# Kernel tuning notes

Hardware: AMD Instinct MI355X
Metric: run time of the kernel (lower is better)

Reference implementation:

```python
import jax, jax.numpy as jnp
import numpy as np

# Model dims (match init_kwargs)
D_OUT = 64      # d_in == d_out
SEQ_L = 4096    # input_len
K_EIG = 24      # num_eigh
K_U = 3         # auto_reg_k_u
K_Y = 2         # auto_reg_k_y
BATCH = 8


def get_top_hankel_eigh(n, k):
    """Top-k eigenpairs of the Hankel matrix Z[i,j] = 2/((i+j)^3-(i+j)), 1-indexed."""
    idx = np.arange(1, n + 1, dtype=np.float64)
    s = idx[:, None] + idx[None, :]
    z = 2.0 / (s ** 3 - s)
    vals, vecs = np.linalg.eigh(z)  # ascending
    return (jnp.asarray(vals[-k:], jnp.float32),        # [k]
            jnp.asarray(vecs[:, -k:], jnp.float32))     # [n, k]


def setup_inputs() -> dict:
    key = jax.random.key(0)
    k1, k2, k3, k4 = jax.random.split(key, 4)
    eig_vals, eig_vecs = get_top_hankel_eigh(SEQ_L, K_EIG)
    m_x_var = 1.0 / float(D_OUT) ** 0.5
    return {
        "inputs": jax.random.normal(k1, (BATCH, SEQ_L, D_OUT), jnp.float32),
        "m_y": jax.random.normal(k2, (D_OUT, K_Y, D_OUT), jnp.float32) * 0.01,
        "m_u": jax.random.normal(k3, (D_OUT, D_OUT, K_U), jnp.float32) * m_x_var,
        "m_phi": jax.random.normal(k4, (D_OUT * K_EIG, D_OUT), jnp.float32) * 0.01,
        "eig_vals": eig_vals,
        "eig_vecs": eig_vecs,
    }


def _stu_single(x, m_y, m_u, m_phi, eig_vals, eig_vecs):
    """apply_stu for one sequence x: [L, d] -> [L, d]."""
    L, d = x.shape
    n = 2 * L
    # --- compute_x_tilde: causal FFT conv of each eigenvector with each channel ---
    V = jnp.fft.rfft(eig_vecs, n=n, axis=0)             # [F, k]
    U = jnp.fft.rfft(x, n=n, axis=0)                    # [F, d]
    xt = jnp.fft.irfft(V[:, :, None] * U[:, None, :], n=n, axis=0)[:L]  # [L, k, d]
    xt = xt * (eig_vals ** 0.25)[None, :, None]
    x_tilde = xt.reshape(L, K_EIG * d)                  # [L, k*d]
    # --- delta_phi ---
    delta_phi = jnp.einsum('lk,kd->ld', x_tilde, m_phi)  # [L, d_out]
    # --- compute_ar_x_preds: shifted AR input contributions ---
    o = jnp.einsum('oik,li->klo', m_u, x)               # [k_u, L, d_out]
    shifts = jnp.arange(K_U)
    o = jax.vmap(lambda a, i: jnp.roll(a, i, axis=0))(o, shifts)
    mask = (jnp.arange(L)[None, :] >= shifts[:, None]).astype(x.dtype)  # [k_u, L]
    delta_ar_u = jnp.sum(o * mask[:, :, None], axis=0)  # [L, d_out]
    deltas = delta_phi + delta_ar_u
    # --- compute_y_t: sequential AR recurrence over time ---
    def step(carry, dlt):  # carry: [k_y, d_out]
        out = jnp.tensordot(m_y, carry, axes=2) + dlt    # [d_out]
        carry = jnp.roll(carry, 1, axis=0).at[0].set(out)
        return carry, out
    _, ys = jax.lax.scan(step, jnp.zeros((K_Y, d), x.dtype), deltas)
    return ys  # [L, d_out]


def reference(inputs, m_y, m_u, m_phi, eig_vals, eig_vecs):
    return jax.vmap(lambda x: _stu_single(x, m_y, m_u, m_phi, eig_vals, eig_vecs))(inputs)
```

## Files before the change

kernel.cpp:

```cpp
#include <hip/hip_runtime.h>
#include <math.h>

#define BB 8
#define LL 4096
#define DD 64
#define KK 24
#define KT 27
#define NN 8192
#define LOGN 13
#define NP 4128
#define NCH 256
#define CH 16
#define PAD 80

typedef unsigned int uint;
typedef unsigned short u16;
typedef __attribute__((ext_vector_type(8))) short bf16x8;
typedef __attribute__((ext_vector_type(4))) float f32x4;

__device__ __forceinline__ float bfl(uint u) {
    union { uint u; float f; } v; v.u = u << 16; return v.f;
}
__device__ __forceinline__ float bfh(uint u) {
    union { uint u; float f; } v; v.u = u & 0xFFFF0000u; return v.f;
}
__device__ __forceinline__ uint pk(float x) {
    union { float f; uint u; } v; v.f = x;
    return (v.u + 0x7FFFu + ((v.u >> 16) & 1u)) >> 16;
}
__device__ __forceinline__ float2 unpk2(uint u) {
    return make_float2(bfl(u), bfh(u));
}
__device__ __forceinline__ int br13(int v) { return (int)(__brev((uint)v) >> 19); }

template<int NT>
__device__ __forceinline__ void build_tw(float2* twc) {
    const int tid = threadIdx.x;
    for (int i = tid; i < 8192; i += NT) {
        if (i == 0) { twc[0] = make_float2(1.f, 0.f); continue; }
        int lh = 31 - __builtin_clz((uint)i);
        int j = i - (1 << lh);
        float ang = -6.28318530717958647692f * (float)j / (float)(2 << lh);
        float sn, cs;
        __sincosf(ang, &sn, &cs);
        twc[i] = make_float2(cs, sn);
    }
}

template<int NT>
__device__ __forceinline__ void fft_dif(float2* a, const float2* __restrict__ twc) {
    const int tid = threadIdx.x;
    for (int lh = LOGN - 1; lh >= 0; --lh) {
        const int half = 1 << lh;
#pragma unroll
        for (int bb = 0; bb < NN / 2 / NT; ++bb) {
            int t = tid + bb * NT;
            int j = t & (half - 1);
            int i0 = ((t >> lh) << (lh + 1)) + j;
            float2 u = a[i0], v = a[i0 + half];
            float2 w = twc[half + j];
            float cs = w.x, sn = w.y;
            float dx = u.x - v.x, dy = u.y - v.y;
            a[i0] = make_float2(u.x + v.x, u.y + v.y);
            a[i0 + half] = make_float2(dx * cs - dy * sn, dx * sn + dy * cs);
        }
        __syncthreads();
    }
}

template<int NT>
__device__ __forceinline__ void fft_dit(float2* a, const float2* __restrict__ twc) {
    const int tid = threadIdx.x;
    for (int lh = 0; lh < LOGN; ++lh) {
        const int half = 1 << lh;
#pragma unroll
        for (int bb = 0; bb < NN / 2 / NT; ++bb) {
            int t = tid + bb * NT;
            int j = t & (half - 1);
            int i0 = ((t >> lh) << (lh + 1)) + j;
            float2 u = a[i0], v = a[i0 + half];
            float2 w = twc[half + j];
            float cs = w.x, sn = -w.y;
            float wx = v.x * cs - v.y * sn;
            float wy = v.x * sn + v.y * cs;
            a[i0] = make_float2(u.x + wx, u.y + wy);
            a[i0 + half] = make_float2(u.x - wx, u.y - wy);
        }
        __syncthreads();
    }
}


__global__ __launch_bounds__(256) void k_pack(const float* __restrict__ mphi,
                                              const float* __restrict__ mu,
                                              uint* __restrict__ mp2) {
    int idx = blockIdx.x * 256 + threadIdx.x;
    if (idx >= KT * 2048) return;
    int k = idx >> 11;
    int rem = idx & 2047;
    int o = rem >> 5, cp = rem & 31;
    int c = cp * 2;
    uint v;
    if (k < KK) {
        v = pk(mphi[(k * 64 + c) * 64 + o]) | (pk(mphi[(k * 64 + c + 1) * 64 + o]) << 16);
    } else {
        int ku = k - KK;
        v = pk(mu[(o * 64 + c) * 3 + ku]) | (pk(mu[(o * 64 + c + 1) * 3 + ku]) << 16);
    }
    mp2[idx] = v;
}

__global__ __launch_bounds__(256) void k_fft_filters(const float* __restrict__ eig_vals,
                                                     const float* __restrict__ eig_vecs,
                                                     float2* __restrict__ Vb) {
    __shared__ float2 a[NN];
    __shared__ float2 twc[8192];
    const int k = blockIdx.x, tid = threadIdx.x;
    const float alpha = powf(eig_vals[k], 0.25f) * (1.0f / (float)NN);
    for (int t = tid; t < LL; t += 256)
        a[t] = make_float2(eig_vecs[t * KK + k] * alpha, 0.f);
    for (int t = LL + tid; t < NN; t += 256)
        a[t] = make_float2(0.f, 0.f);
    build_tw<256>(twc);
    __syncthreads();
    fft_dif<256>(a, twc);
    for (int r = tid; r < NN; r += 256)
        Vb[(size_t)r * KK + k] = a[r];
}

__global__ __launch_bounds__(512) void k_fft_x2(const float* __restrict__ x,
                                                uint* __restrict__ Uxp,
                                                uint* __restrict__ Uyp) {
    __shared__ float2 a[NN];
    __shared__ float2 twc[8192];
    const int b = blockIdx.x & 7, cp = blockIdx.x >> 3;
    const int tid = threadIdx.x;
    for (int l = tid; l < LL; l += 512)
        a[l] = *(const float2*)&x[((size_t)b * LL + l) * DD + 2 * cp];
    for (int l = LL + tid; l < NN; l += 512)
        a[l] = make_float2(0.f, 0.f);
    build_tw<512>(twc);
    __syncthreads();
    fft_dif<512>(a, twc);
    const size_t plane = ((size_t)b * 32 + cp) * NP;
    for (int idx = tid; idx < 4097; idx += 512) {
        int r = (idx == 4096) ? 1 : 2 * idx;
        int fn = br13(r);
        int q = br13((8192 - fn) & 8191);
        float2 Z = a[r], W = a[q];
        float ucx = 0.5f * (Z.x + W.x), ucy = 0.5f * (Z.y - W.y);
        float upx = 0.5f * (Z.y + W.y), upy = 0.5f * (W.x - Z.x);
        Uxp[plane + idx] = pk(ucx) | (pk(upx) << 16);
        Uyp[plane + idx] = pk(ucy) | (pk(upy) << 16);
    }
    for (int idx = 4097 + tid; idx < NP; idx += 512) {
        Uxp[plane + idx] = 0;
        Uyp[plane + idx] = 0;
    }
}

__global__ __launch_bounds__(256) void k_modulate5(const float2* __restrict__ Vb,
                                                   const uint* __restrict__ Uxp,
                                                   const uint* __restrict__ Uyp,
                                                   const uint* __restrict__ mp2,
                                                   uint* __restrict__ Sb2) {
    __shared__ u16 Uxs[32][PAD];
    __shared__ u16 Uys[32][PAD];
    __shared__ u16 mpT[2][64][PAD];
    __shared__ float2 Vt[32][28];
    const int tid = threadIdx.x;
    const int pt = blockIdx.x;
    const int b  = blockIdx.y;
    const int p0 = pt * 32;

    for (int i = tid; i < 1024; i += 256) {
        int cp = i >> 5, row = i & 31;
        uint vx = Uxp[((size_t)b * 32 + cp) * NP + p0 + row];
        uint vy = Uyp[((size_t)b * 32 + cp) * NP + p0 + row];
        *(uint*)&Uxs[row][cp * 2] = vx;
        *(uint*)&Uys[row][cp * 2] = vy;
    }
    {
        int o = tid >> 2, seg = tid & 3;
        const uint4* src = (const uint4*)&mp2[(size_t)o * 32 + seg * 8];
        uint4 m0 = src[0], m1 = src[1];
        *(uint4*)&mpT[0][o][seg * 16] = m0;
        *(uint4*)&mpT[0][o][seg * 16 + 8] = m1;
    }
    for (int i = tid; i < 768; i += 256) {
        int pi = i / 24, kk = i - pi * 24;
        int pidx = p0 + pi; if (pidx > 4096) pidx = 4096;
        int r = (pidx == 4096) ? 1 : 2 * pidx;
        Vt[pi][kk] = Vb[(size_t)r * KK + kk];
    }
    for (int pi = tid; pi < 32; pi += 256) {
        int pidx = p0 + pi; if (pidx > 4096) pidx = 4096;
        int r = (pidx == 4096) ? 1 : 2 * pidx;
        int f = br13(r);
        const float invN = 1.f / 8192.f;
        float ph = -6.28318530717958647692f * (float)f * invN;
        float s1, c1, s2, c2;
        __sincosf(ph, &s1, &c1);
        __sincosf(2.f * ph, &s2, &c2);
        Vt[pi][24] = make_float2(invN, 0.f);
        Vt[pi][25] = make_float2(c1 * invN, s1 * invN);
        Vt[pi][26] = make_float2(c2 * invN, s2 * invN);
    }
    __syncthreads();

    const int lane = tid & 63, w = tid >> 6;
    const int rt = w & 1, chalf = w >> 1;
    const int lrow = lane & 15, lk = lane >> 4;
    const u16* axp = &Uxs[rt * 16 + lrow][lk * 8];
    const u16* ayp = &Uys[rt * 16 + lrow][lk * 8];

    float Sx0[4] = {0.f, 0.f, 0.f, 0.f}, Sy0[4] = {0.f, 0.f, 0.f, 0.f};
    float Sx1[4] = {0.f, 0.f, 0.f, 0.f}, Sy1[4] = {0.f, 0.f, 0.f, 0.f};

    for (int k = 0; k < KT; ++k) {
        const int cur = k & 1;
        bf16x8 ax0 = *(const bf16x8*)(axp);
        bf16x8 ax1 = *(const bf16x8*)(axp + 32);
        bf16x8 ay0 = *(const bf16x8*)(ayp);
        bf16x8 ay1 = *(const bf16x8*)(ayp + 32);
        const u16* bp0 = &mpT[cur][chalf * 32 + lrow][lk * 8];
        const u16* bp1 = &mpT[cur][chalf * 32 + 16 + lrow][lk * 8];
        bf16x8 b00 = *(const bf16x8*)(bp0);
        bf16x8 b01 = *(const bf16x8*)(bp0 + 32);
        bf16x8 b10 = *(const bf16x8*)(bp1);
        bf16x8 b11 = *(const bf16x8*)(bp1 + 32);
        float2 v0 = Vt[rt * 16 + lk * 4 + 0][k];
        float2 v1 = Vt[rt * 16 + lk * 4 + 1][k];
        float2 v2 = Vt[rt * 16 + lk * 4 + 2][k];
        float2 v3 = Vt[rt * 16 + lk * 4 + 3][k];
        if (k + 1 < KT) {
            int o = tid >> 2, seg = tid & 3;
            const uint4* src = (const uint4*)&mp2[((size_t)(k + 1) * 64 + o) * 32 + seg * 8];
            uint4 m0 = src[0], m1 = src[1];
            *(uint4*)&mpT[cur ^ 1][o][seg * 16] = m0;
            *(uint4*)&mpT[cur ^ 1][o][seg * 16 + 8] = m1;
        }
        f32x4 z = {0.f, 0.f, 0.f, 0.f};
        f32x4 Wx0 = __builtin_amdgcn_mfma_f32_16x16x32_bf16(ax0, b00, z, 0, 0, 0);
        Wx0 = __builtin_amdgcn_mfma_f32_16x16x32_bf16(ax1, b01, Wx0, 0, 0, 0);
        f32x4 Wy0 = __builtin_amdgcn_mfma_f32_16x16x32_bf16(ay0, b00, z, 0, 0, 0);
        Wy0 = __builtin_amdgcn_mfma_f32_16x16x32_bf16(ay1, b01, Wy0, 0, 0, 0);
        f32x4 Wx1 = __builtin_amdgcn_mfma_f32_16x16x32_bf16(ax0, b10, z, 0, 0, 0);
        Wx1 = __builtin_amdgcn_mfma_f32_16x16x32_bf16(ax1, b11, Wx1, 0, 0, 0);
        f32x4 Wy1 = __builtin_amdgcn_mfma_f32_16x16x32_bf16(ay0, b10, z, 0, 0, 0);
        Wy1 = __builtin_amdgcn_mfma_f32_16x16x32_bf16(ay1, b11, Wy1, 0, 0, 0);
        Sx0[0] += v0.x * Wx0[0] - v0.y * Wy0[0];  Sy0[0] += v0.x * Wy0[0] + v0.y * Wx0[0];
        Sx0[1] += v1.x * Wx0[1] - v1.y * Wy0[1];  Sy0[1] += v1.x * Wy0[1] + v1.y * Wx0[1];
        Sx0[2] += v2.x * Wx0[2] - v2.y * Wy0[2];  Sy0[2] += v2.x * Wy0[2] + v2.y * Wx0[2];
        Sx0[3] += v3.x * Wx0[3] - v3.y * Wy0[3];  Sy0[3] += v3.x * Wy0[3] + v3.y * Wx0[3];
        Sx1[0] += v0.x * Wx1[0] - v0.y * Wy1[0];  Sy1[0] += v0.x * Wy1[0] + v0.y * Wx1[0];
        Sx1[1] += v1.x * Wx1[1] - v1.y * Wy1[1];  Sy1[1] += v1.x * Wy1[1] + v1.y * Wx1[1];
        Sx1[2] += v2.x * Wx1[2] - v2.y * Wy1[2];  Sy1[2] += v2.x * Wy1[2] + v2.y * Wx1[2];
        Sx1[3] += v3.x * Wx1[3] - v3.y * Wy1[3];  Sy1[3] += v3.x * Wy1[3] + v3.y * Wx1[3];
        __syncthreads();
    }
    const int rbase = rt * 16 + lk * 4;
    const int o0 = chalf * 32 + lrow;
    const size_t pl0 = ((size_t)b * 64 + o0) * NP + p0 + rbase;
    const size_t pl1 = ((size_t)b * 64 + o0 + 16) * NP + p0 + rbase;
#pragma unroll
    for (int j = 0; j < 4; ++j) {
        Sb2[pl0 + j] = pk(Sx0[j]) | (pk(Sy0[j]) << 16);
        Sb2[pl1 + j] = pk(Sx1[j]) | (pk(Sy1[j]) << 16);
    }
}

__global__ __launch_bounds__(512) void k_ifft2(const uint* __restrict__ Sb2,
                                               float* __restrict__ deltas) {
    __shared__ float2 a[NN];
    __shared__ float2 twc[8192];
    const int b = blockIdx.x & 7, op = blockIdx.x >> 3;
    const int tid = threadIdx.x;
    const uint* s0 = &Sb2[((size_t)b * 64 + op * 2) * NP];
    const uint* s1 = &Sb2[((size_t)b * 64 + op * 2 + 1) * NP];
    for (int idx = tid; idx < 4097; idx += 512) {
        int r = (idx == 4096) ? 1 : 2 * idx;
        float2 A = unpk2(s0[idx]), B = unpk2(s1[idx]);
        a[r] = make_float2(A.x - B.y, A.y + B.x);
        int fn = br13(r);
        int q = br13((8192 - fn) & 8191);
        if (q != r) a[q] = make_float2(A.x + B.y, B.x - A.y);
    }
    build_tw<512>(twc);
    __syncthreads();
    fft_dit<512>(a, twc);
    float* d0 = &deltas[((size_t)b * 64 + op * 2) * LL];
    float* d1 = &deltas[((size_t)b * 64 + op * 2 + 1) * LL];
    for (int l = tid; l < LL; l += 512) {
        d0[l] = a[l].x;
        d1[l] = a[l].y;
    }
}

__global__ __launch_bounds__(256) void k_matsq1(const float* __restrict__ m_y,
                                                float* __restrict__ C) {
    int idx = blockIdx.x * 256 + threadIdx.x;
    int r = idx >> 7, c = idx & 127;
    if (r >= 64) { C[idx] = m_y[(r - 64) * 128 + c]; return; }
    float acc = (c < 64) ? m_y[r * 128 + 64 + c] : 0.f;
#pragma unroll
    for (int i = 0; i < 64; ++i) acc += m_y[r * 128 + i] * m_y[i * 128 + c];
    C[idx] = acc;
}

__global__ __launch_bounds__(256) void k_matsq(const float* __restrict__ A,
                                               float* __restrict__ C) {
    int idx = blockIdx.x * 256 + threadIdx.x;
    int r = idx >> 7, c = idx & 127;
    float acc = 0.f;
#pragma unroll
    for (int i = 0; i < 128; ++i) acc += A[r * 128 + i] * A[i * 128 + c];
    C[idx] = acc;
}

__device__ __forceinline__ void load_rowhalf(const float* __restrict__ P, int r, int h,
                                             float* __restrict__ p) {
#pragma unroll
    for (int i4 = 0; i4 < 16; ++i4) {
        float4 v = *(const float4*)&P[r * 128 + h * 64 + i4 * 4];
        p[4 * i4] = v.x; p[4 * i4 + 1] = v.y; p[4 * i4 + 2] = v.z; p[4 * i4 + 3] = v.w;
    }
}
__device__ __forceinline__ float dot64(const float* __restrict__ p, const float* s) {
    float a0 = 0.f, a1 = 0.f, a2 = 0.f, a3 = 0.f;
#pragma unroll
    for (int i4 = 0; i4 < 16; ++i4) {
        float4 w = *(const float4*)&s[i4 * 4];
        a0 += p[4 * i4] * w.x;  a1 += p[4 * i4 + 1] * w.y;
        a2 += p[4 * i4 + 2] * w.z;  a3 += p[4 * i4 + 3] * w.w;
    }
    return (a0 + a1) + (a2 + a3);
}

__global__ __launch_bounds__(256, 1) void k_scan(const float* __restrict__ P,
                                                 const float* __restrict__ in,
                                                 float* __restrict__ partial,
                                                 float* __restrict__ terminal,
                                                 const int count) {
    const int bx = blockIdx.x;
    const int tid = threadIdx.x;
    const int r = tid & 127, h = tid >> 7;
    __shared__ __align__(16) float scur[128];
    __shared__ float pacc[256];
    float p[64];
    load_rowhalf(P, r, h, p);
    if (tid < 128) scur[tid] = 0.f;
    __syncthreads();
    const size_t base = (size_t)bx * count * 128;
    for (int k = 0; k < count; ++k) {
        if (tid < 128) partial[base + (size_t)k * 128 + tid] = scur[tid];
        pacc[tid] = dot64(p, &scur[h * 64]);
        __syncthreads();
        if (tid < 128) scur[tid] = pacc[tid] + pacc[tid + 128] + in[base + (size_t)k * 128 + tid];
        __syncthreads();
    }
    if (tid < 128) terminal[(size_t)bx * 128 + tid] = scur[tid];
}

__global__ __launch_bounds__(256, 1) void k_fixupg(const float* __restrict__ P,
                                                   const float* __restrict__ Sinit,
                                                   const float* __restrict__ q,
                                                   float* __restrict__ out,
                                                   const int count) {
    const int bx = blockIdx.x;
    const int tid = threadIdx.x;
    const int r = tid & 127, h = tid >> 7;
    __shared__ __align__(16) float scur[128];
    __shared__ float pacc[256];
    float p[64];
    load_rowhalf(P, r, h, p);
    if (tid < 128) scur[tid] = Sinit[(size_t)bx * 128 + tid];
    __syncthreads();
    const size_t base = (size_t)bx * count * 128;
    for (int k = 0; k < count; ++k) {
        if (tid < 128) out[base + (size_t)k * 128 + tid] = scur[tid] + q[base + (size_t)k * 128 + tid];
        if (k == count - 1) break;
        pacc[tid] = dot64(p, &scur[h * 64]);
        __syncthreads();
        if (tid < 128) scur[tid] = pacc[tid] + pacc[tid + 128];
        __syncthreads();
    }
}

__global__ __launch_bounds__(128, 1) void k_chunk_local(const float* __restrict__ deltas,
                                                        const float* __restrict__ m_y,
                                                        float* __restrict__ term) {
    const int b = blockIdx.x >> 8, j = blockIdx.x & 255;
    const int tid = threadIdx.x;
    const int o = tid & 63, h = tid >> 6;
    __shared__ __align__(16) float y1s[64];
    __shared__ __align__(16) float y2s[64];
    __shared__ float pacc[128];
    float m1[32], m2[32];
#pragma unroll
    for (int i4 = 0; i4 < 8; ++i4) {
        float4 v1 = *(const float4*)&m_y[o * 128 + h * 32 + i4 * 4];
        float4 v2 = *(const float4*)&m_y[o * 128 + 64 + h * 32 + i4 * 4];
        m1[4 * i4] = v1.x; m1[4 * i4 + 1] = v1.y; m1[4 * i4 + 2] = v1.z; m1[4 * i4 + 3] = v1.w;
        m2[4 * i4] = v2.x; m2[4 * i4 + 1] = v2.y; m2[4 * i4 + 2] = v2.z; m2[4 * i4 + 3] = v2.w;
    }
    if (tid < 64) { y1s[tid] = 0.f; y2s[tid] = 0.f; }
    __syncthreads();
    const float* dl = &deltas[((size_t)b * 64 + o) * LL + j * CH];
    for (int t = 0; t < CH; ++t) {
        float a0 = 0.f, a1 = 0.f, a2 = 0.f, a3 = 0.f;
#pragma unroll
        for (int i4 = 0; i4 < 8; ++i4) {
            float4 w1 = *(const float4*)&y1s[h * 32 + i4 * 4];
            float4 w2 = *(const float4*)&y2s[h * 32 + i4 * 4];
            a0 += m1[4 * i4] * w1.x + m2[4 * i4] * w2.x;
            a1 += m1[4 * i4 + 1] * w1.y + m2[4 * i4 + 1] * w2.y;
            a2 += m1[4 * i4 + 2] * w1.z + m2[4 * i4 + 2] * w2.z;
            a3 += m1[4 * i4 + 3] * w1.w + m2[4 * i4 + 3] * w2.w;
        }
        pacc[tid] = (a0 + a1) + (a2 + a3);
        __syncthreads();
        if (h == 0) {
            float outv = pacc[o] + pacc[o + 64] + dl[t];
            y2s[o] = y1s[o];
            y1s[o] = outv;
        }
        __syncthreads();
    }
    if (tid < 64) {
        term[((size_t)b * NCH + j) * 128 + o] = y1s[o];
        term[((size_t)b * NCH + j) * 128 + 64 + o] = y2s[o];
    }
}

__global__ __launch_bounds__(128, 1) void k_chunk_final(const float* __restrict__ deltas,
                                                        const float* __restrict__ m_y,
                                                        const float* __restrict__ sstate,
                                                        float* __restrict__ out) {
    const int b = blockIdx.x >> 8, j = blockIdx.x & 255;
    const int tid = threadIdx.x;
    const int o = tid & 63, h = tid >> 6;
    __shared__ __align__(16) float y1s[64];
    __shared__ __align__(16) float y2s[64];
    __shared__ float pacc[128];
    float m1[32], m2[32];
#pragma unroll
    for (int i4 = 0; i4 < 8; ++i4) {
        float4 v1 = *(const float4*)&m_y[o * 128 + h * 32 + i4 * 4];
        float4 v2 = *(const float4*)&m_y[o * 128 + 64 + h * 32 + i4 * 4];
        m1[4 * i4] = v1.x; m1[4 * i4 + 1] = v1.y; m1[4 * i4 + 2] = v1.z; m1[4 * i4 + 3] = v1.w;
        m2[4 * i4] = v2.x; m2[4 * i4 + 1] = v2.y; m2[4 * i4 + 2] = v2.z; m2[4 * i4 + 3] = v2.w;
    }
    if (tid < 64) {
        y1s[tid] = sstate[((size_t)b * NCH + j) * 128 + tid];
        y2s[tid] = sstate[((size_t)b * NCH + j) * 128 + 64 + tid];
    }
    __syncthreads();
    const float* dl = &deltas[((size_t)b * 64 + o) * LL + j * CH];
    const size_t obase = (((size_t)b * LL) + j * CH) * DD + o;
    for (int t = 0; t < CH; ++t) {
        float a0 = 0.f, a1 = 0.f, a2 = 0.f, a3 = 0.f;
#pragma unroll
        for (int i4 = 0; i4 < 8; ++i4) {
            float4 w1 = *(const float4*)&y1s[h * 32 + i4 * 4];
            float4 w2 = *(const float4*)&y2s[h * 32 + i4 * 4];
            a0 += m1[4 * i4] * w1.x + m2[4 * i4] * w2.x;
            a1 += m1[4 * i4 + 1] * w1.y + m2[4 * i4 + 1] * w2.y;
            a2 += m1[4 * i4 + 2] * w1.z + m2[4 * i4 + 2] * w2.z;
            a3 += m1[4 * i4 + 3] * w1.w + m2[4 * i4 + 3] * w2.w;
        }
        pacc[tid] = (a0 + a1) + (a2 + a3);
        __syncthreads();
        if (h == 0) {
            float outv = pacc[o] + pacc[o + 64] + dl[t];
            out[obase + (size_t)t * DD] = outv;
            y2s[o] = y1s[o];
            y1s[o] = outv;
        }
        __syncthreads();
    }
}

extern "C" void kernel_launch(void* const* d_in, const int* in_sizes, int n_in,
                              void* d_out, int out_size, void* d_ws, size_t ws_size,
                              hipStream_t stream) {
    const float* x        = (const float*)d_in[0];
    const float* m_y      = (const float*)d_in[1];
    const float* m_u      = (const float*)d_in[2];
    const float* m_phi    = (const float*)d_in[3];
    const float* eig_vals = (const float*)d_in[4];
    const float* eig_vecs = (const float*)d_in[5];
    float* out = (float*)d_out;

    char* ws = (char*)d_ws;
    size_t off = 0;
    auto alloc = [&](size_t bytes) -> void* {
        void* p = ws + off;
        off += (bytes + 255) & ~(size_t)255;
        return p;
    };
    float2* Vb   = (float2*)alloc((size_t)NN * KK * sizeof(float2));
    uint*   Uxp  = (uint*)alloc((size_t)BB * 32 * NP * sizeof(uint));
    uint*   Uyp  = (uint*)alloc((size_t)BB * 32 * NP * sizeof(uint));
    uint*   Sb2  = (uint*)alloc((size_t)BB * 64 * NP * sizeof(uint));
    float*  deltas = (float*)alloc((size_t)BB * 64 * LL * sizeof(float));
    uint*   mp2  = (uint*)alloc((size_t)KT * 64 * 32 * sizeof(uint));
    float*  mats = (float*)alloc((size_t)5 * 128 * 128 * sizeof(float));
    float*  term = (float*)alloc((size_t)BB * NCH * 128 * sizeof(float));
    float*  sst  = (float*)alloc((size_t)BB * NCH * 128 * sizeof(float));
    float*  qbuf = (float*)alloc((size_t)BB * NCH * 128 * sizeof(float));
    float*  Qg   = (float*)alloc((size_t)BB * 32 * 128 * sizeof(float));
    float*  q2   = (float*)alloc((size_t)BB * 32 * 128 * sizeof(float));
    float*  Sgt  = (float*)alloc((size_t)BB * 32 * 128 * sizeof(float));
    float*  Qsg  = (float*)alloc((size_t)BB * 4 * 128 * sizeof(float));
    float*  Ssg  = (float*)alloc((size_t)BB * 4 * 128 * sizeof(float));
    float*  dmy  = (float*)alloc((size_t)8 * 128 * sizeof(float));

    k_pack<<<dim3(216), dim3(256), 0, stream>>>(m_phi, m_u, mp2);
    k_fft_filters<<<dim3(24), dim3(256), 0, stream>>>(eig_vals, eig_vecs, Vb);
    k_fft_x2<<<dim3(256), dim3(512), 0, stream>>>(x, Uxp, Uyp);

    float* T1    = mats;
    float* T2    = mats + 16384;
    float* P16   = mats + 32768;
    float* P128  = mats + 49152;
    float* P1024 = mats + 65536;
    k_matsq1<<<dim3(64), dim3(256), 0, stream>>>(m_y, T1);
    k_matsq<<<dim3(64), dim3(256), 0, stream>>>(T1, T2);
    k_matsq<<<dim3(64), dim3(256), 0, stream>>>(T2, T1);
    k_matsq<<<dim3(64), dim3(256), 0, stream>>>(T1, P16);
    k_matsq<<<dim3(64), dim3(256), 0, stream>>>(P16, T1);
    k_matsq<<<dim3(64), dim3(256), 0, stream>>>(T1, T2);
    k_matsq<<<dim3(64), dim3(256), 0, stream>>>(T2, P128);
    k_matsq<<<dim3(64), dim3(256), 0, stream>>>(P128, T1);
    k_matsq<<<dim3(64), dim3(256), 0, stream>>>(T1, T2);
    k_matsq<<<dim3(64), dim3(256), 0, stream>>>(T2, P1024);

    k_modulate5<<<dim3(129, 8), dim3(256), 0, stream>>>(Vb, Uxp, Uyp, mp2, Sb2);
    k_ifft2<<<dim3(256), dim3(512), 0, stream>>>(Sb2, deltas);

    k_chunk_local<<<dim3(2048), dim3(128), 0, stream>>>(deltas, m_y, term);
    k_scan<<<dim3(256), dim3(256), 0, stream>>>(P16, term, qbuf, Qg, 8);
    k_scan<<<dim3(32), dim3(256), 0, stream>>>(P128, Qg, q2, Qsg, 8);
    k_scan<<<dim3(8), dim3(256), 0, stream>>>(P1024, Qsg, Ssg, dmy, 4);
    k_fixupg<<<dim3(32), dim3(256), 0, stream>>>(P128, Ssg, q2, Sgt, 8);
    k_fixupg<<<dim3(256), dim3(256), 0, stream>>>(P16, Sgt, qbuf, sst, 8);
    k_chunk_final<<<dim3(2048), dim3(128), 0, stream>>>(deltas, m_y, sst, out);
}
```

Before: 240.1 us.

## Precompute FFT twiddles globally and flatten scan hierarchy to two levels

```diff
diff --git a/kernel.cpp b/kernel.cpp
--- a/kernel.cpp
+++ b/kernel.cpp
@@ -33,18 +33,16 @@
 }
 __device__ __forceinline__ int br13(int v) { return (int)(__brev((uint)v) >> 19); }
 
-template<int NT>
-__device__ __forceinline__ void build_tw(float2* twc) {
-    const int tid = threadIdx.x;
-    for (int i = tid; i < 8192; i += NT) {
-        if (i == 0) { twc[0] = make_float2(1.f, 0.f); continue; }
-        int lh = 31 - __builtin_clz((uint)i);
-        int j = i - (1 << lh);
-        float ang = -6.28318530717958647692f * (float)j / (float)(2 << lh);
-        float sn, cs;
-        __sincosf(ang, &sn, &cs);
-        twc[i] = make_float2(cs, sn);
-    }
+__global__ __launch_bounds__(512) void k_twiddle(float2* __restrict__ twc) {
+    int i = blockIdx.x * 512 + threadIdx.x;
+    if (i >= 8192) return;
+    if (i == 0) { twc[0] = make_float2(1.f, 0.f); return; }
+    int lh = 31 - __builtin_clz((uint)i);
+    int j = i - (1 << lh);
+    float ang = -6.28318530717958647692f * (float)j / (float)(2 << lh);
+    float sn, cs;
+    __sincosf(ang, &sn, &cs);
+    twc[i] = make_float2(cs, sn);
 }
 
 template<int NT>
@@ -112,16 +110,15 @@
 
 __global__ __launch_bounds__(256) void k_fft_filters(const float* __restrict__ eig_vals,
                                                      const float* __restrict__ eig_vecs,
+                                                     const float2* __restrict__ twc,
                                                      float2* __restrict__ Vb) {
     __shared__ float2 a[NN];
-    __shared__ float2 twc[8192];
     const int k = blockIdx.x, tid = threadIdx.x;
     const float alpha = powf(eig_vals[k], 0.25f) * (1.0f / (float)NN);
     for (int t = tid; t < LL; t += 256)
         a[t] = make_float2(eig_vecs[t * KK + k] * alpha, 0.f);
     for (int t = LL + tid; t < NN; t += 256)
         a[t] = make_float2(0.f, 0.f);
-    build_tw<256>(twc);
     __syncthreads();
     fft_dif<256>(a, twc);
     for (int r = tid; r < NN; r += 256)
@@ -129,17 +126,16 @@
 }
 
 __global__ __launch_bounds__(512) void k_fft_x2(const float* __restrict__ x,
+                                                const float2* __restrict__ twc,
                                                 uint* __restrict__ Uxp,
                                                 uint* __restrict__ Uyp) {
     __shared__ float2 a[NN];
-    __shared__ float2 twc[8192];
     const int b = blockIdx.x & 7, cp = blockIdx.x >> 3;
     const int tid = threadIdx.x;
     for (int l = tid; l < LL; l += 512)
         a[l] = *(const float2*)&x[((size_t)b * LL + l) * DD + 2 * cp];
     for (int l = LL + tid; l < NN; l += 512)
         a[l] = make_float2(0.f, 0.f);
-    build_tw<512>(twc);
     __syncthreads();
     fft_dif<512>(a, twc);
     const size_t plane = ((size_t)b * 32 + cp) * NP;
@@ -271,9 +267,9 @@
 }
 
 __global__ __launch_bounds__(512) void k_ifft2(const uint* __restrict__ Sb2,
+                                               const float2* __restrict__ twc,
                                                float* __restrict__ deltas) {
     __shared__ float2 a[NN];
-    __shared__ float2 twc[8192];
     const int b = blockIdx.x & 7, op = blockIdx.x >> 3;
     const int tid = threadIdx.x;
     const uint* s0 = &Sb2[((size_t)b * 64 + op * 2) * NP];
@@ -286,7 +282,6 @@
         int q = br13((8192 - fn) & 8191);
         if (q != r) a[q] = make_float2(A.x + B.y, B.x - A.y);
     }
-    build_tw<512>(twc);
     __syncthreads();
     fft_dit<512>(a, twc);
     float* d0 = &deltas[((size_t)b * 64 + op * 2) * LL];
@@ -505,45 +500,39 @@
     uint*   Sb2  = (uint*)alloc((size_t)BB * 64 * NP * sizeof(uint));
     float*  deltas = (float*)alloc((size_t)BB * 64 * LL * sizeof(float));
     uint*   mp2  = (uint*)alloc((size_t)KT * 64 * 32 * sizeof(uint));
-    float*  mats = (float*)alloc((size_t)5 * 128 * 128 * sizeof(float));
+    float2* twcg = (float2*)alloc((size_t)8192 * sizeof(float2));
+    float*  mats = (float*)alloc((size_t)4 * 128 * 128 * sizeof(float));
     float*  term = (float*)alloc((size_t)BB * NCH * 128 * sizeof(float));
     float*  sst  = (float*)alloc((size_t)BB * NCH * 128 * sizeof(float));
     float*  qbuf = (float*)alloc((size_t)BB * NCH * 128 * sizeof(float));
-    float*  Qg   = (float*)alloc((size_t)BB * 32 * 128 * sizeof(float));
-    float*  q2   = (float*)alloc((size_t)BB * 32 * 128 * sizeof(float));
-    float*  Sgt  = (float*)alloc((size_t)BB * 32 * 128 * sizeof(float));
-    float*  Qsg  = (float*)alloc((size_t)BB * 4 * 128 * sizeof(float));
-    float*  Ssg  = (float*)alloc((size_t)BB * 4 * 128 * sizeof(float));
+    float*  Qg   = (float*)alloc((size_t)BB * 16 * 128 * sizeof(float));
+    float*  Sgt  = (float*)alloc((size_t)BB * 16 * 128 * sizeof(float));
     float*  dmy  = (float*)alloc((size_t)8 * 128 * sizeof(float));
 
+    k_twiddle<<<dim3(16), dim3(512), 0, stream>>>(twcg);
     k_pack<<<dim3(216), dim3(256), 0, stream>>>(m_phi, m_u, mp2);
-    k_fft_filters<<<dim3(24), dim3(256), 0, stream>>>(eig_vals, eig_vecs, Vb);
-    k_fft_x2<<<dim3(256), dim3(512), 0, stream>>>(x, Uxp, Uyp);
-
-    float* T1    = mats;
-    float* T2    = mats + 16384;
-    float* P16   = mats + 32768;
-    float* P128  = mats + 49152;
-    float* P1024 = mats + 65536;
+    k_fft_filters<<<dim3(24), dim3(256), 0, stream>>>(eig_vals, eig_vecs, twcg, Vb);
+    k_fft_x2<<<dim3(256), dim3(512), 0, stream>>>(x, twcg, Uxp, Uyp);
+
+    float* T1   = mats;
+    float* T2   = mats + 16384;
+    float* P16  = mats + 32768;
+    float* P256 = mats + 49152;
     k_matsq1<<<dim3(64), dim3(256), 0, stream>>>(m_y, T1);
     k_matsq<<<dim3(64), dim3(256), 0, stream>>>(T1, T2);
     k_matsq<<<dim3(64), dim3(256), 0, stream>>>(T2, T1);
     k_matsq<<<dim3(64), dim3(256), 0, stream>>>(T1, P16);
     k_matsq<<<dim3(64), dim3(256), 0, stream>>>(P16, T1);
     k_matsq<<<dim3(64), dim3(256), 0, stream>>>(T1, T2);
-    k_matsq<<<dim3(64), dim3(256), 0, stream>>>(T2, P128);
-    k_matsq<<<dim3(64), dim3(256), 0, stream>>>(P128, T1);
-    k_matsq<<<dim3(64), dim3(256), 0, stream>>>(T1, T2);
-    k_matsq<<<dim3(64), dim3(256), 0, stream>>>(T2, P1024);
+    k_matsq<<<dim3(64), dim3(256), 0, stream>>>(T2, T1);
+    k_matsq<<<dim3(64), dim3(256), 0, stream>>>(T1, P256);
 
     k_modulate5<<<dim3(129, 8), dim3(256), 0, stream>>>(Vb, Uxp, Uyp, mp2, Sb2);
-    k_ifft2<<<dim3(256), dim3(512), 0, stream>>>(Sb2, deltas);
+    k_ifft2<<<dim3(256), dim3(512), 0, stream>>>(Sb2, twcg, deltas);
 
     k_chunk_local<<<dim3(2048), dim3(128), 0, stream>>>(deltas, m_y, term);
-    k_scan<<<dim3(256), dim3(256), 0, stream>>>(P16, term, qbuf, Qg, 8);
-    k_scan<<<dim3(32), dim3(256), 0, stream>>>(P128, Qg, q2, Qsg, 8);
-    k_scan<<<dim3(8), dim3(256), 0, stream>>>(P1024, Qsg, Ssg, dmy, 4);
-    k_fixupg<<<dim3(32), dim3(256), 0, stream>>>(P128, Ssg, q2, Sgt, 8);
-    k_fixupg<<<dim3(256), dim3(256), 0, stream>>>(P16, Sgt, qbuf, sst, 8);
+    k_scan<<<dim3(128), dim3(256), 0, stream>>>(P16, term, qbuf, Qg, 16);
+    k_scan<<<dim3(8), dim3(256), 0, stream>>>(P256, Qg, Sgt, dmy, 16);
+    k_fixupg<<<dim3(128), dim3(256), 0, stream>>>(P16, Sgt, qbuf, sst, 16);
     k_chunk_final<<<dim3(2048), dim3(128), 0, stream>>>(deltas, m_y, sst, out);
 }
```

Measured after the change: 240.7 us. About the same (+0.2%).
